# Performance work log

Hardware: AMD Instinct MI355X
Metric: run time of the kernel (lower is better)

## Reference

```python
import jax, jax.numpy as jnp
import numpy as np

NUM_PROB_BINS = 15
NUM_CLASSES = 8
NEIGHBORHOOD_WIDTH = 3
NUM_NEIGHBOR_CLASSES = NEIGHBORHOOD_WIDTH ** 2  # 9
B, H, W = 16, 512, 512


def _bin_index(x, nbins):
    # Uniform bins on [0, 1]: bin_idx = floor(x * nbins), last bin closed at 1.0.
    idx = jnp.floor(x * nbins).astype(jnp.int32)
    return jnp.clip(idx, 0, nbins - 1)


def setup_inputs() -> dict:
    key = jax.random.key(0)
    k1, k2 = jax.random.split(key)
    logits = jax.random.normal(k1, (B, NUM_CLASSES, H, W), dtype=jnp.float32)
    # Precomputed calibration frequency table: [num_classes, num_neighbor_bins, num_prob_bins]
    val_freqs = jax.random.uniform(k2, (NUM_CLASSES, NUM_NEIGHBOR_CLASSES, NUM_PROB_BINS), dtype=jnp.float32)
    return {"logits": logits, "val_freqs": val_freqs}


def reference(logits, val_freqs):
    probs = jax.nn.softmax(logits, axis=1)  # [B, C, H, W]
    kw = NEIGHBORHOOD_WIDTH
    # agg_neighbors_preds (soft, class_wise): mean prob over kw x kw spatial neighborhood.
    neigh_mean = jax.lax.reduce_window(
        probs, 0.0, jax.lax.add,
        window_dimensions=(1, 1, kw, kw),
        window_strides=(1, 1, 1, 1),
        padding='SAME',
    ) / float(kw * kw)
    loc_bin = _bin_index(neigh_mean, NUM_NEIGHBOR_CLASSES)  # [B,C,H,W] int32 in [0,9)
    prob_bin = _bin_index(probs, NUM_PROB_BINS)             # [B,C,H,W] int32 in [0,15)
    # The nested class/neighbor-bin loops + masked assignment collapse to one fused gather:
    cls_idx = jnp.arange(NUM_CLASSES, dtype=jnp.int32)[None, :, None, None]
    calibrated = val_freqs[cls_idx, loc_bin, prob_bin]       # [B,C,H,W]
    # normalize=True branch
    s = jnp.sum(calibrated, axis=1, keepdims=True)
    s = jnp.where(s == 0, jnp.ones_like(s), s)
    return calibrated / s
```

## Files before the change

kernel.cpp:

```cpp
#include <hip/hip_runtime.h>
#include <math.h>

constexpr int NPB = 15;
constexpr int NC  = 8;
constexpr int NNB = 9;
constexpr int Bn  = 16;
constexpr int Hc  = 512;
constexpr int Wc  = 512;

constexpr int TX = 32, TY = 32;
constexpr int HX = TX + 2;
constexpr int HY = TY + 2;
constexpr int NT = 512;
constexpr int GX = Wc / TX;
constexpr int GY = Hc / TY;
constexpr int NBLK = GX * GY * Bn;

__device__ __forceinline__ float exp_f32_cr(float df) {
    const double d = (double)df;
    double t  = d * 2.8853900817779268;
    double kd = rint(t);
    int    k  = (int)kd;
    double r  = fma(kd, -0.34657359027997265, d);
    double p = 2.48015873015873016e-5;
    p = fma(p, r, 1.98412698412698413e-4);
    p = fma(p, r, 1.38888888888888889e-3);
    p = fma(p, r, 8.33333333333333333e-3);
    p = fma(p, r, 4.16666666666666666e-2);
    p = fma(p, r, 1.66666666666666667e-1);
    p = fma(p, r, 0.5);
    p = fma(p, r, 1.0);
    p = fma(p, r, 1.0);
    double v = (k & 1) ? p * 1.4142135623730951 : p;
    long long bits = __double_as_longlong(v) + ((long long)(k >> 1) << 52);
    return (float)__longlong_as_double(bits);
}

__device__ __forceinline__ double rcp64(float s) {
    double dS = (double)s;
    double r  = (double)__builtin_amdgcn_rcpf(s);
    r = r * fma(-dS, r, 2.0);
    r = r * fma(-dS, r, 2.0);
    return r;
}

__global__ __launch_bounds__(NT)
void nectar_kernel(const float* __restrict__ logits,
                   const float* __restrict__ vf,
                   float* __restrict__ out)
{
    __shared__ float sP[NC][HY][HX];
    __shared__ float sVF[NC * NNB * NPB];

    const int tid = threadIdx.x;

    const int h    = blockIdx.x;
    const int sg   = h >> 8;
    const int xcd  = h & 7;
    const int slot = (h >> 3) & 31;
    const int sem  = (sg << 8) + (xcd << 5) + slot;

    const int bx = sem & (GX - 1);
    const int by = (sem >> 4) & (GY - 1);
    const int b  = sem >> 8;
    const int x0 = bx * TX;
    const int y0 = by * TY;

    for (int i = tid; i < NC * NNB * NPB; i += NT) sVF[i] = vf[i];

    const size_t plane = (size_t)Hc * Wc;
    const float* src = logits + (size_t)b * NC * plane;

    for (int i = tid; i < HX * HY; i += NT) {
        const int ly = i / HX;
        const int lx = i - ly * HX;
        const int gy = y0 + ly - 1;
        const int gx = x0 + lx - 1;
        if ((unsigned)gy < (unsigned)Hc && (unsigned)gx < (unsigned)Wc) {
            const float* p = src + (size_t)gy * Wc + gx;
            float v[NC];
            #pragma unroll
            for (int c = 0; c < NC; c++) v[c] = p[(size_t)c * plane];
            float m = v[0];
            #pragma unroll
            for (int c = 1; c < NC; c++) m = fmaxf(m, v[c]);
            float S = 0.0f;
            #pragma unroll
            for (int c = 0; c < NC; c++) {
                v[c] = exp_f32_cr(v[c] - m);
                S = S + v[c];
            }
            double rS = rcp64(S);
            #pragma unroll
            for (int c = 0; c < NC; c++)
                sP[c][ly][lx] = (float)((double)v[c] * rS);
        } else {
            #pragma unroll
            for (int c = 0; c < NC; c++) sP[c][ly][lx] = 0.0f;
        }
    }
    __syncthreads();

    const int lx  = tid & (TX - 1);
    const int oy0 = (tid >> 5) * 2;
    const int gx  = x0 + lx;
    const int gy0 = y0 + oy0;

    const double C9 = 0.1111111111111111111;

    float cal0[NC], cal1[NC];
    float s0 = 0.0f, s1 = 0.0f;
    #pragma unroll
    for (int c = 0; c < NC; c++) {
        float r0a = sP[c][oy0 + 0][lx], r0b = sP[c][oy0 + 0][lx + 1], r0c = sP[c][oy0 + 0][lx + 2];
        float r1a = sP[c][oy0 + 1][lx], r1b = sP[c][oy0 + 1][lx + 1], r1c = sP[c][oy0 + 1][lx + 2];
        float r2a = sP[c][oy0 + 2][lx], r2b = sP[c][oy0 + 2][lx + 1], r2c = sP[c][oy0 + 2][lx + 2];
        float r3a = sP[c][oy0 + 3][lx], r3b = sP[c][oy0 + 3][lx + 1], r3c = sP[c][oy0 + 3][lx + 2];
        float a0 = ((((((((r0a + r0b) + r0c) + r1a) + r1b) + r1c) + r2a) + r2b) + r2c);
        float a1 = ((((((((r1a + r1b) + r1c) + r2a) + r2b) + r2c) + r3a) + r3b) + r3c);

        float nm0 = (float)((double)a0 * C9);
        float nm1 = (float)((double)a1 * C9);
        int lb0 = (int)(nm0 * 9.0f);
        int lb1 = (int)(nm1 * 9.0f);
        lb0 = lb0 > NNB - 1 ? NNB - 1 : lb0;
        lb1 = lb1 > NNB - 1 ? NNB - 1 : lb1;
        int pb0 = (int)(r1b * 15.0f);
        int pb1 = (int)(r2b * 15.0f);
        pb0 = pb0 > NPB - 1 ? NPB - 1 : pb0;
        pb1 = pb1 > NPB - 1 ? NPB - 1 : pb1;
        cal0[c] = sVF[(c * NNB + lb0) * NPB + pb0];
        cal1[c] = sVF[(c * NNB + lb1) * NPB + pb1];
        s0 = s0 + cal0[c];
        s1 = s1 + cal1[c];
    }
    if (s0 == 0.0f) s0 = 1.0f;
    if (s1 == 0.0f) s1 = 1.0f;

    float q0 = __builtin_amdgcn_rcpf(s0);
    q0 = q0 * fmaf(-s0, q0, 2.0f);
    float q1 = __builtin_amdgcn_rcpf(s1);
    q1 = q1 * fmaf(-s1, q1, 2.0f);

    float* dst = out + (size_t)b * NC * plane + (size_t)gy0 * Wc + gx;
    #pragma unroll
    for (int c = 0; c < NC; c++) {
        dst[(size_t)c * plane]      = cal0[c] * q0;
        dst[(size_t)c * plane + Wc] = cal1[c] * q1;
    }
}

extern "C" void kernel_launch(void* const* d_in, const int* in_sizes, int n_in,
                              void* d_out, int out_size, void* d_ws, size_t ws_size,
                              hipStream_t stream) {
    const float* logits = (const float*)d_in[0];
    const float* vf     = (const float*)d_in[1];
    float* out          = (float*)d_out;

    nectar_kernel<<<dim3(NBLK), dim3(NT), 0, stream>>>(logits, vf, out);
}
```

Baseline: 239.5 us.

## Widen tiles to 64x32 with horizontal pixel pairs, vector LDS loads and nontemporal stores

The tile grows to 64x32 with 1024 threads, and each thread now handles two horizontally adjacent pixels instead of two vertically adjacent ones. The 3x3 neighbourhood is read with 2-wide LDS loads and the outputs are written as float2 nontemporal stores. The larger tile lowers the fraction of halo recomputation (softmax on border pixels) and the pairing gives coalesced 8-byte global stores. The risks are fewer blocks per CU due to the larger block and shared memory size, possible misaligned f32x2 LDS reads since HX=66 with even offsets, and a block remap that must still cover all tiles.

After: 235.8 us. No clear change (-1.5%).

```diff
diff --git a/kernel.cpp b/kernel.cpp
--- a/kernel.cpp
+++ b/kernel.cpp
@@ -8,13 +8,15 @@
 constexpr int Hc  = 512;
 constexpr int Wc  = 512;
 
-constexpr int TX = 32, TY = 32;
+constexpr int TX = 64, TY = 32;
 constexpr int HX = TX + 2;
 constexpr int HY = TY + 2;
-constexpr int NT = 512;
+constexpr int NT = 1024;
 constexpr int GX = Wc / TX;
 constexpr int GY = Hc / TY;
 constexpr int NBLK = GX * GY * Bn;
+
+typedef float f32x2 __attribute__((ext_vector_type(2)));
 
 __device__ __forceinline__ float exp_f32_cr(float df) {
     const double d = (double)df;
@@ -44,12 +46,12 @@
     return r;
 }
 
-__global__ __launch_bounds__(NT)
+__global__ __launch_bounds__(NT, 8)
 void nectar_kernel(const float* __restrict__ logits,
                    const float* __restrict__ vf,
                    float* __restrict__ out)
 {
-    __shared__ float sP[NC][HY][HX];
+    __shared__ __align__(16) float sP[NC][HY][HX];
     __shared__ float sVF[NC * NNB * NPB];
 
     const int tid = threadIdx.x;
@@ -61,8 +63,8 @@
     const int sem  = (sg << 8) + (xcd << 5) + slot;
 
     const int bx = sem & (GX - 1);
-    const int by = (sem >> 4) & (GY - 1);
-    const int b  = sem >> 8;
+    const int by = (sem >> 3) & (GY - 1);
+    const int b  = sem >> 7;
     const int x0 = bx * TX;
     const int y0 = by * TY;
 
@@ -101,23 +103,26 @@
     }
     __syncthreads();
 
-    const int lx  = tid & (TX - 1);
-    const int oy0 = (tid >> 5) * 2;
-    const int gx  = x0 + lx;
-    const int gy0 = y0 + oy0;
+    const int lx2 = (tid & 31) * 2;
+    const int oy  = tid >> 5;
+    const int gx2 = x0 + lx2;
+    const int gy  = y0 + oy;
 
     const double C9 = 0.1111111111111111111;
 
-    float cal0[NC], cal1[NC];
+    float calL[NC], calR[NC];
     float s0 = 0.0f, s1 = 0.0f;
     #pragma unroll
     for (int c = 0; c < NC; c++) {
-        float r0a = sP[c][oy0 + 0][lx], r0b = sP[c][oy0 + 0][lx + 1], r0c = sP[c][oy0 + 0][lx + 2];
-        float r1a = sP[c][oy0 + 1][lx], r1b = sP[c][oy0 + 1][lx + 1], r1c = sP[c][oy0 + 1][lx + 2];
-        float r2a = sP[c][oy0 + 2][lx], r2b = sP[c][oy0 + 2][lx + 1], r2c = sP[c][oy0 + 2][lx + 2];
-        float r3a = sP[c][oy0 + 3][lx], r3b = sP[c][oy0 + 3][lx + 1], r3c = sP[c][oy0 + 3][lx + 2];
-        float a0 = ((((((((r0a + r0b) + r0c) + r1a) + r1b) + r1c) + r2a) + r2b) + r2c);
-        float a1 = ((((((((r1a + r1b) + r1c) + r2a) + r2b) + r2c) + r3a) + r3b) + r3c);
+        const float* base = &sP[c][oy][lx2];
+        f32x2 u0 = *(const f32x2*)(base);
+        f32x2 v0 = *(const f32x2*)(base + 2);
+        f32x2 u1 = *(const f32x2*)(base + HX);
+        f32x2 v1 = *(const f32x2*)(base + HX + 2);
+        f32x2 u2 = *(const f32x2*)(base + 2 * HX);
+        f32x2 v2 = *(const f32x2*)(base + 2 * HX + 2);
+        float a0 = ((((((((u0.x + u0.y) + v0.x) + u1.x) + u1.y) + v1.x) + u2.x) + u2.y) + v2.x);
+        float a1 = ((((((((u0.y + v0.x) + v0.y) + u1.y) + v1.x) + v1.y) + u2.y) + v2.x) + v2.y);
 
         float nm0 = (float)((double)a0 * C9);
         float nm1 = (float)((double)a1 * C9);
@@ -125,14 +130,14 @@
         int lb1 = (int)(nm1 * 9.0f);
         lb0 = lb0 > NNB - 1 ? NNB - 1 : lb0;
         lb1 = lb1 > NNB - 1 ? NNB - 1 : lb1;
-        int pb0 = (int)(r1b * 15.0f);
-        int pb1 = (int)(r2b * 15.0f);
+        int pb0 = (int)(u1.y * 15.0f);
+        int pb1 = (int)(v1.x * 15.0f);
         pb0 = pb0 > NPB - 1 ? NPB - 1 : pb0;
         pb1 = pb1 > NPB - 1 ? NPB - 1 : pb1;
-        cal0[c] = sVF[(c * NNB + lb0) * NPB + pb0];
-        cal1[c] = sVF[(c * NNB + lb1) * NPB + pb1];
-        s0 = s0 + cal0[c];
-        s1 = s1 + cal1[c];
+        calL[c] = sVF[(c * NNB + lb0) * NPB + pb0];
+        calR[c] = sVF[(c * NNB + lb1) * NPB + pb1];
+        s0 = s0 + calL[c];
+        s1 = s1 + calR[c];
     }
     if (s0 == 0.0f) s0 = 1.0f;
     if (s1 == 0.0f) s1 = 1.0f;
@@ -142,11 +147,13 @@
     float q1 = __builtin_amdgcn_rcpf(s1);
     q1 = q1 * fmaf(-s1, q1, 2.0f);
 
-    float* dst = out + (size_t)b * NC * plane + (size_t)gy0 * Wc + gx;
+    float* dst = out + (size_t)b * NC * plane + (size_t)gy * Wc + gx2;
     #pragma unroll
     for (int c = 0; c < NC; c++) {
-        dst[(size_t)c * plane]      = cal0[c] * q0;
-        dst[(size_t)c * plane + Wc] = cal1[c] * q1;
+        f32x2 o;
+        o.x = calL[c] * q0;
+        o.y = calR[c] * q1;
+        __builtin_nontemporal_store(o, (f32x2*)(dst + (size_t)c * plane));
     }
 }
 
```
